# Kernel tuning notes

Measured on AMD Instinct MI355X. Metric: run time of the kernel, lower is better.

The kernel has to match this reference:

```python
import jax, jax.numpy as jnp
import numpy as np

NUM_EXPERTS = 8
IN_FEATURES = 1024
HIDDEN_FEATURES = 4096
OUT_FEATURES = 1024
TOKENS = 8192


def setup_inputs() -> dict:
    key = jax.random.key(0)
    k_x, k_idx, k_w1, k_w2, k_b1, k_b2 = jax.random.split(key, 6)
    x = jax.random.normal(k_x, (TOKENS, IN_FEATURES), dtype=jnp.float32)
    indices_s = jax.random.randint(k_idx, (TOKENS,), 0, NUM_EXPERTS, dtype=jnp.int64)
    # learned parameters (torch uses torch.rand; scaled for numeric sanity)
    weight1 = jax.random.normal(k_w1, (NUM_EXPERTS, IN_FEATURES, HIDDEN_FEATURES), dtype=jnp.float32) * 0.02
    weight2 = jax.random.normal(k_w2, (NUM_EXPERTS, HIDDEN_FEATURES, OUT_FEATURES), dtype=jnp.float32) * 0.02
    bias1 = jax.random.normal(k_b1, (NUM_EXPERTS, HIDDEN_FEATURES), dtype=jnp.float32) * 0.02
    bias2 = jax.random.normal(k_b2, (NUM_EXPERTS, IN_FEATURES), dtype=jnp.float32) * 0.02
    return {"x": x, "indices_s": indices_s, "weight1": weight1, "weight2": weight2, "bias1": bias1, "bias2": bias2}


def reference(x, indices_s, weight1, weight2, bias1, bias2):
    # Per-token expert MLP. Rather than gathering full weight matrices per
    # token (weight[indices_s] -> [T, in, hid], huge), loop over the small
    # fixed expert set and mask-combine. Math identical to the torch module.
    T = x.shape[0]
    num_experts = weight1.shape[0]
    out = jnp.zeros((T, weight2.shape[2]), dtype=x.dtype)
    for e in range(num_experts):
        mask = (indices_s == e)[:, None]  # [T, 1]
        h = jax.nn.gelu(x @ weight1[e] + bias1[e], approximate=False)  # [T, hid]
        y = h @ weight2[e] + bias2[e]  # [T, out]
        out = out + jnp.where(mask, y, jnp.zeros((), dtype=x.dtype))
    # original returns shape [T, 1, out] (x was unsqueezed)
    return out[:, None, :]
```

## Files before the change

kernel.cpp:

```cpp
#include <hip/hip_runtime.h>
#include <hip/hip_bf16.h>
#include <math.h>

#define TOKENS 8192
#define IN_F   1024
#define HID_F  4096
#define OUT_F  1024
#define NEXP   8
#define TSLOTS 40

typedef __attribute__((ext_vector_type(8))) short bf16x8;
typedef __attribute__((ext_vector_type(4))) float f32x4;
typedef __attribute__((ext_vector_type(8))) unsigned short u16x8;

__device__ __forceinline__ unsigned short f2bf(float f) {
    unsigned int u = __float_as_uint(f);
    u += 0x7fffu + ((u >> 16) & 1u);
    return (unsigned short)(u >> 16);
}

__device__ __forceinline__ void gload_lds16(const unsigned short* g, unsigned char* lds) {
    __builtin_amdgcn_global_load_lds(
        (const __attribute__((address_space(1))) void*)g,
        (__attribute__((address_space(3))) void*)lds, 16, 0, 0);
}

__global__ void sort_kernel(const int* __restrict__ idx, int* __restrict__ perm,
                            int* __restrict__ off, int* __restrict__ table) {
    __shared__ int cnt[NEXP];
    __shared__ int base[NEXP];
    const int tid = threadIdx.x, lane = tid & 63;
    if (tid < NEXP) cnt[tid] = 0;
    __syncthreads();
    for (int i = tid; i < TOKENS; i += 1024) {
        int e = idx[i];
#pragma unroll
        for (int ex = 0; ex < NEXP; ++ex) {
            unsigned long long m = __ballot(e == ex);
            if (lane == 0 && m) atomicAdd(&cnt[ex], __popcll(m));
        }
    }
    __syncthreads();
    if (tid == 0) {
        int s = 0;
        for (int e = 0; e < NEXP; ++e) { off[e] = s; base[e] = s; s += cnt[e]; }
        off[NEXP] = s;
        int t = 0;
        for (int e = 0; e < NEXP; ++e)
            for (int m0 = off[e]; m0 < off[e + 1]; m0 += 256)
                table[t++] = (e << 13) | m0;
        for (; t < TSLOTS; ++t) table[t] = -1;
    }
    __syncthreads();
    for (int i = tid; i < TOKENS; i += 1024) {
        int e = idx[i];
#pragma unroll
        for (int ex = 0; ex < NEXP; ++ex) {
            unsigned long long m = __ballot(e == ex);
            if (e == ex) {
                int lead = (int)__ffsll((long long)m) - 1;
                int pos = 0;
                if (lane == lead) pos = atomicAdd(&base[ex], __popcll(m));
                pos = __shfl(pos, lead);
                pos += __popcll(m & ((1ULL << lane) - 1ULL));
                perm[pos] = i;
            }
        }
    }
}

__device__ __forceinline__ void transp_tile(const float* __restrict__ in,
                                            unsigned short* __restrict__ out,
                                            int R, int C, int e, int by, int bx,
                                            unsigned short* T, int st) {
    const int r0 = by * 64, c0 = bx * 64;
    const int rr = st >> 4, cc = st & 15;
    const float* ip = in + ((size_t)e * R + r0) * C + c0;
#pragma unroll
    for (int p = 0; p < 4; ++p) {
        int r = p * 16 + rr;
        float4 v = *(const float4*)(ip + (size_t)r * C + cc * 4);
        T[(cc * 4 + 0) * 65 + r] = f2bf(v.x);
        T[(cc * 4 + 1) * 65 + r] = f2bf(v.y);
        T[(cc * 4 + 2) * 65 + r] = f2bf(v.z);
        T[(cc * 4 + 3) * 65 + r] = f2bf(v.w);
    }
    __syncthreads();
    unsigned short* op = out + ((size_t)e * C + c0) * R + r0;
    const int c = st >> 2, ch = st & 3;
    u16x8 a, b;
#pragma unroll
    for (int i = 0; i < 8; ++i) a[i] = T[c * 65 + ch * 16 + i];
#pragma unroll
    for (int i = 0; i < 8; ++i) b[i] = T[c * 65 + ch * 16 + 8 + i];
    *(u16x8*)(op + (size_t)c * R + ch * 16) = a;
    *(u16x8*)(op + (size_t)c * R + ch * 16 + 8) = b;
}

__global__ void transp(const float* __restrict__ in, unsigned short* __restrict__ out,
                       int R, int C) {
    __shared__ unsigned short T[64 * 65];
    transp_tile(in, out, R, C, blockIdx.z, blockIdx.y, blockIdx.x, T, threadIdx.x);
}

__global__ void fused_pre(const float* __restrict__ x, const int* __restrict__ perm,
                          unsigned short* __restrict__ xg,
                          const float* __restrict__ w1, unsigned short* __restrict__ w1t) {
    __shared__ unsigned short T[64 * 65];
    const int bid = blockIdx.x, t = threadIdx.x;
    if (bid < TOKENS) {
        const int src = perm[bid];
        float4 v = *(const float4*)(x + (size_t)src * IN_F + t * 4);
        unsigned long long pk =
            (unsigned long long)f2bf(v.x) |
            ((unsigned long long)f2bf(v.y) << 16) |
            ((unsigned long long)f2bf(v.z) << 32) |
            ((unsigned long long)f2bf(v.w) << 48);
        *(unsigned long long*)(xg + (size_t)bid * IN_F + t * 4) = pk;
        return;
    }
    const int id = bid - TOKENS;
    const int e = id >> 10, rem = id & 1023;
    const int by = rem >> 6, bx = rem & 63;
    transp_tile(w1, w1t, IN_F, HID_F, e, by, bx, T, t);
}

#define RD_A(RB, HALF) \
  _Pragma("unroll") for (int m_ = 0; m_ < 4; ++m_) { \
    const int row_ = wr * 128 + (HALF) * 64 + m_ * 16 + lr; \
    _Pragma("unroll") for (int kk_ = 0; kk_ < 2; ++kk_) \
      aR[m_][kk_] = *(const bf16x8*)((RB) + row_ * 128 + (((kk_ * 4 + hk) << 4) ^ xorc)); }

#define RD_B(RB, NH, DST) \
  _Pragma("unroll") for (int nn_ = 0; nn_ < 2; ++nn_) { \
    const int row_ = wc * 64 + ((NH) * 2 + nn_) * 16 + lr; \
    _Pragma("unroll") for (int kk_ = 0; kk_ < 2; ++kk_) \
      DST[nn_][kk_] = *(const bf16x8*)((RB) + 32768 + row_ * 128 + (((kk_ * 4 + hk) << 4) ^ xorc)); }

#define MFMA_Q(MH, NH, B) \
  __builtin_amdgcn_s_setprio(1); \
  _Pragma("unroll") for (int m_ = 0; m_ < 4; ++m_) \
    _Pragma("unroll") for (int nn_ = 0; nn_ < 2; ++nn_) \
      _Pragma("unroll") for (int kk_ = 0; kk_ < 2; ++kk_) \
        acc[(MH) * 4 + m_][(NH) * 2 + nn_] = __builtin_amdgcn_mfma_f32_16x16x32_bf16( \
            aR[m_][kk_], B[nn_][kk_], acc[(MH) * 4 + m_][(NH) * 2 + nn_], 0, 0, 0); \
  __builtin_amdgcn_s_setprio(0);

template<int K, int ND, bool GELU>
__launch_bounds__(512, 2)
__global__ void moe_gemm8p(const unsigned short* __restrict__ A,
                           const unsigned short* __restrict__ W,
                           const float* __restrict__ bias,
                           const int* __restrict__ perm,
                           const int* __restrict__ off,
                           const int* __restrict__ table,
                           void* __restrict__ outp,
                           const float* __restrict__ w2src,
                           unsigned short* __restrict__ w2t) {
    const int nwg = (ND / 256) * TSLOTS;

    __shared__ __align__(16) unsigned char L[131072];
    const int tid = threadIdx.x;

    if ((int)blockIdx.x >= nwg) {
        const int sub = tid >> 8, st = tid & 255;
        const int id2 = ((int)blockIdx.x - nwg) * 2 + sub;
        const int e = id2 >> 10, rem = id2 & 1023;
        const int by = rem >> 4, bx = rem & 15;
        unsigned short* T = (unsigned short*)(L + sub * 8448);
        transp_tile(w2src, w2t, HID_F, OUT_F, e, by, bx, T, st);
        return;
    }

    const int chunk = nwg >> 3;
    const int logical = ((int)blockIdx.x & 7) * chunk + ((int)blockIdx.x >> 3);
    const int nt = logical / TSLOTS;
    const int ts = logical - nt * TSLOTS;
    const int te = table[ts];
    if (te < 0) return;
    const int e  = te >> 13;
    const int m0 = te & 8191;
    const int sege = off[e + 1];
    const int n0 = nt * 256;

    const int wid = tid >> 6, lane = tid & 63;
    const int wr = wid >> 2, wc = wid & 3;
    const int lr = lane & 15, hk = lane >> 4;

    const unsigned short* We = W + (size_t)e * ND * K + (size_t)n0 * K;

    const int srow8 = lane >> 3;
    const int sch   = (lane & 7) ^ srow8;
    const unsigned short* aSrc[4];
    const unsigned short* wSrc[4];
#pragma unroll
    for (int cc = 0; cc < 4; ++cc) {
        int rt = cc * 64 + wid * 8 + srow8;
        int ga = m0 + rt; if (ga > TOKENS - 1) ga = TOKENS - 1;
        aSrc[cc] = A  + (size_t)ga * K + sch * 8;
        wSrc[cc] = We + (size_t)rt * K + sch * 8;
    }
    const int dstBase = wid * 1024;

    constexpr int NT = K / 64;

    auto stageH = [&](int tile, int h) {
        const int buf = (tile & 1) * 65536;
        const int op  = (h >> 1) * 32768;
        const int c0_ = (h & 1) * 2;
        const int ko  = tile * 64;
#pragma unroll
        for (int j = 0; j < 2; ++j) {
            int cc = c0_ + j;
            const unsigned short* s = (h < 2) ? (aSrc[cc] + ko) : (wSrc[cc] + ko);
            gload_lds16(s, L + buf + op + cc * 8192 + dstBase);
        }
    };

    f32x4 acc[8][4];
#pragma unroll
    for (int i = 0; i < 8; ++i)
#pragma unroll
        for (int j = 0; j < 4; ++j) acc[i][j] = (f32x4){0.f, 0.f, 0.f, 0.f};

    bf16x8 aR[4][2], b0R[2][2], b1R[2][2];
    const int xorc = (lr & 7) << 4;
    const unsigned char* rb0 = L;
    const unsigned char* rb1 = L + 65536;

    stageH(0, 0); stageH(0, 1); stageH(0, 2); stageH(0, 3);
    stageH(1, 0);
    asm volatile("s_waitcnt vmcnt(2)" ::: "memory");
    __builtin_amdgcn_s_barrier();
    __builtin_amdgcn_sched_barrier(0);

#pragma unroll 1
    for (int i = 0; i < NT / 2; ++i) {
        const int T1 = 2 * i + 1;
        const bool lastIt = (i == NT / 2 - 1);
        RD_A(rb0, 0); RD_B(rb0, 0, b0R);
        stageH(T1, 1);
        __builtin_amdgcn_s_barrier();
        MFMA_Q(0, 0, b0R);
        __builtin_amdgcn_s_barrier();
        RD_B(rb0, 1, b1R);
        stageH(T1, 2);
        __builtin_amdgcn_s_barrier();
        MFMA_Q(0, 1, b1R);
        __builtin_amdgcn_s_barrier();
        RD_A(rb0, 1);
        stageH(T1, 3);
        __builtin_amdgcn_s_barrier();
        MFMA_Q(1, 1, b1R);
        __builtin_amdgcn_s_barrier();
        if (!lastIt) stageH(T1 + 1, 0);
        __builtin_amdgcn_s_barrier();
        MFMA_Q(1, 0, b0R);
        if (lastIt) { asm volatile("s_waitcnt vmcnt(0)" ::: "memory"); }
        else        { asm volatile("s_waitcnt vmcnt(2)" ::: "memory"); }
        __builtin_amdgcn_s_barrier();
        __builtin_amdgcn_sched_barrier(0);
        RD_A(rb1, 0); RD_B(rb1, 0, b0R);
        if (!lastIt) stageH(T1 + 1, 1);
        __builtin_amdgcn_s_barrier();
        MFMA_Q(0, 0, b0R);
        __builtin_amdgcn_s_barrier();
        RD_B(rb1, 1, b1R);
        if (!lastIt) stageH(T1 + 1, 2);
        __builtin_amdgcn_s_barrier();
        MFMA_Q(0, 1, b1R);
        __builtin_amdgcn_s_barrier();
        RD_A(rb1, 1);
        if (!lastIt) stageH(T1 + 1, 3);
        __builtin_amdgcn_s_barrier();
        MFMA_Q(1, 1, b1R);
        __builtin_amdgcn_s_barrier();
        if (!lastIt) stageH(T1 + 2, 0);
        __builtin_amdgcn_s_barrier();
        MFMA_Q(1, 0, b0R);
        if (!lastIt) { asm volatile("s_waitcnt vmcnt(2)" ::: "memory"); }
        __builtin_amdgcn_s_barrier();
        __builtin_amdgcn_sched_barrier(0);
    }

    const float* be = bias + (size_t)e * ND + n0;
#pragma unroll
    for (int m = 0; m < 8; ++m) {
#pragma unroll
        for (int r = 0; r < 4; ++r) {
            int row = wr * 128 + m * 16 + hk * 4 + r;
            int grow = m0 + row;
            if (grow >= sege) continue;
            if constexpr (GELU) {
                unsigned short* h = (unsigned short*)outp;
                size_t base = (size_t)grow * ND + n0;
#pragma unroll
                for (int n = 0; n < 4; ++n) {
                    int col = wc * 64 + n * 16 + lr;
                    float v = acc[m][n][r] + be[col];
                    float u = v * (0.7978845608f + 0.0356774081f * v * v);
                    float g = v / (1.0f + __expf(-2.0f * u));
                    h[base + col] = f2bf(g);
                }
            } else {
                float* out = (float*)outp;
                int tok = perm[grow];
                size_t base = (size_t)tok * ND + n0;
#pragma unroll
                for (int n = 0; n < 4; ++n) {
                    int col = wc * 64 + n * 16 + lr;
                    out[base + col] = acc[m][n][r] + be[col];
                }
            }
        }
    }
}

extern "C" void kernel_launch(void* const* d_in, const int* in_sizes, int n_in,
                              void* d_out, int out_size, void* d_ws, size_t ws_size,
                              hipStream_t stream) {
    const float* x   = (const float*)d_in[0];
    const int*   idx = (const int*)d_in[1];
    const float* w1  = (const float*)d_in[2];
    const float* w2  = (const float*)d_in[3];
    const float* b1  = (const float*)d_in[4];
    const float* b2  = (const float*)d_in[5];
    float* out = (float*)d_out;

    int* perm  = (int*)d_ws;
    int* off   = perm + TOKENS;
    int* table = off + 16;
    unsigned short* xg  = (unsigned short*)((char*)d_ws + 65536);
    unsigned short* h   = xg + (size_t)TOKENS * IN_F;
    unsigned short* w1t = h + (size_t)TOKENS * HID_F;
    unsigned short* w2t = w1t + (size_t)NEXP * IN_F * HID_F;
    const size_t need_fused = 65536
        + (size_t)TOKENS * IN_F * 2
        + (size_t)TOKENS * HID_F * 2
        + (size_t)NEXP * IN_F * HID_F * 2 * 2;
    const bool fused = (ws_size >= need_fused);

    hipLaunchKernelGGL(sort_kernel, dim3(1), dim3(1024), 0, stream, idx, perm, off, table);
    hipLaunchKernelGGL(fused_pre, dim3(TOKENS + NEXP * (IN_F / 64) * (HID_F / 64)),
                       dim3(256), 0, stream, x, perm, xg, w1, w1t);

    const int g1 = (HID_F / 256) * TSLOTS;
    const int t2 = NEXP * (OUT_F / 64) * (HID_F / 64) / 2;
    if (fused) {
        hipLaunchKernelGGL((moe_gemm8p<IN_F, HID_F, true>), dim3(g1 + t2), dim3(512),
                           0, stream, xg, w1t, b1, perm, off, table, (void*)h, w2, w2t);
        hipLaunchKernelGGL((moe_gemm8p<HID_F, OUT_F, false>),
                           dim3((OUT_F / 256) * TSLOTS), dim3(512),
                           0, stream, h, w2t, b2, perm, off, table, (void*)out,
                           (const float*)nullptr, (unsigned short*)nullptr);
    } else {
        hipLaunchKernelGGL((moe_gemm8p<IN_F, HID_F, true>), dim3(g1), dim3(512),
                           0, stream, xg, w1t, b1, perm, off, table, (void*)h,
                           (const float*)nullptr, (unsigned short*)nullptr);
        hipLaunchKernelGGL(transp, dim3(OUT_F / 64, HID_F / 64, NEXP), dim3(256), 0, stream,
                           w2, w1t, HID_F, OUT_F);
        hipLaunchKernelGGL((moe_gemm8p<HID_F, OUT_F, false>),
                           dim3((OUT_F / 256) * TSLOTS), dim3(512),
                           0, stream, h, w1t, b2, perm, off, table, (void*)out,
                           (const float*)nullptr, (unsigned short*)nullptr);
    }
}
```

Before: 320.0 us.

## Merge MoE pipeline into persistent cooperative kernel with grid syncs and smaller GEMM2 tiles

Replaces the separate pre-processing, GEMM1 and GEMM2 launches with one persistent cooperative kernel of 256 workgroups. Each workgroup pulls work items from atomic counters, and grid-wide syncs separate the three phases. GEMM2 moves to 128x128 tiles with a new table, giving more tiles so the work is better balanced across CUs. Launch gaps and tail imbalance shrink, at the cost of occupancy 1 (512 threads, 128KB LDS), grid-sync overhead and lost overlap between phases. A fallback path using standalone kernels runs if the cooperative launch fails.

Result: slower. 797.8 us (+149.3%).

```diff
diff --git a/kernel.cpp b/kernel.cpp
--- a/kernel.cpp
+++ b/kernel.cpp
@@ -1,13 +1,17 @@
 #include <hip/hip_runtime.h>
 #include <hip/hip_bf16.h>
+#include <hip/hip_cooperative_groups.h>
 #include <math.h>
+
+namespace cg = cooperative_groups;
 
 #define TOKENS 8192
 #define IN_F   1024
 #define HID_F  4096
 #define OUT_F  1024
 #define NEXP   8
-#define TSLOTS 40
+#define TSLOTS    40
+#define TSLOTS128 72
 
 typedef __attribute__((ext_vector_type(8))) short bf16x8;
 typedef __attribute__((ext_vector_type(4))) float f32x4;
@@ -26,7 +30,8 @@
 }
 
 __global__ void sort_kernel(const int* __restrict__ idx, int* __restrict__ perm,
-                            int* __restrict__ off, int* __restrict__ table) {
+                            int* __restrict__ off, int* __restrict__ table,
+                            int* __restrict__ table128, int* __restrict__ ctrs) {
     __shared__ int cnt[NEXP];
     __shared__ int base[NEXP];
     const int tid = threadIdx.x, lane = tid & 63;
@@ -50,6 +55,12 @@
             for (int m0 = off[e]; m0 < off[e + 1]; m0 += 256)
                 table[t++] = (e << 13) | m0;
         for (; t < TSLOTS; ++t) table[t] = -1;
+        int t2 = 0;
+        for (int e = 0; e < NEXP; ++e)
+            for (int m0 = off[e]; m0 < off[e + 1]; m0 += 128)
+                table128[t2++] = (e << 13) | m0;
+        for (; t2 < TSLOTS128; ++t2) table128[t2] = -1;
+        ctrs[0] = 0; ctrs[1] = 0; ctrs[2] = 0; ctrs[3] = 0;
     }
     __syncthreads();
     for (int i = tid; i < TOKENS; i += 1024) {
@@ -95,12 +106,6 @@
     for (int i = 0; i < 8; ++i) b[i] = T[c * 65 + ch * 16 + 8 + i];
     *(u16x8*)(op + (size_t)c * R + ch * 16) = a;
     *(u16x8*)(op + (size_t)c * R + ch * 16 + 8) = b;
-}
-
-__global__ void transp(const float* __restrict__ in, unsigned short* __restrict__ out,
-                       int R, int C) {
-    __shared__ unsigned short T[64 * 65];
-    transp_tile(in, out, R, C, blockIdx.z, blockIdx.y, blockIdx.x, T, threadIdx.x);
 }
 
 __global__ void fused_pre(const float* __restrict__ x, const int* __restrict__ perm,
@@ -120,9 +125,7 @@
         return;
     }
     const int id = bid - TOKENS;
-    const int e = id >> 10, rem = id & 1023;
-    const int by = rem >> 6, bx = rem & 63;
-    transp_tile(w1, w1t, IN_F, HID_F, e, by, bx, T, t);
+    transp_tile(w1, w1t, IN_F, HID_F, id >> 10, (id >> 6) & 15, id & 63, T, t);
 }
 
 #define RD_A(RB, HALF) \
@@ -146,49 +149,18 @@
             aR[m_][kk_], B[nn_][kk_], acc[(MH) * 4 + m_][(NH) * 2 + nn_], 0, 0, 0); \
   __builtin_amdgcn_s_setprio(0);
 
-template<int K, int ND, bool GELU>
-__launch_bounds__(512, 2)
-__global__ void moe_gemm8p(const unsigned short* __restrict__ A,
+template<int K, int ND>
+__device__ void gemm1_tile(const unsigned short* __restrict__ A,
                            const unsigned short* __restrict__ W,
                            const float* __restrict__ bias,
-                           const int* __restrict__ perm,
-                           const int* __restrict__ off,
-                           const int* __restrict__ table,
-                           void* __restrict__ outp,
-                           const float* __restrict__ w2src,
-                           unsigned short* __restrict__ w2t) {
-    const int nwg = (ND / 256) * TSLOTS;
-
-    __shared__ __align__(16) unsigned char L[131072];
-    const int tid = threadIdx.x;
-
-    if ((int)blockIdx.x >= nwg) {
-        const int sub = tid >> 8, st = tid & 255;
-        const int id2 = ((int)blockIdx.x - nwg) * 2 + sub;
-        const int e = id2 >> 10, rem = id2 & 1023;
-        const int by = rem >> 4, bx = rem & 15;
-        unsigned short* T = (unsigned short*)(L + sub * 8448);
-        transp_tile(w2src, w2t, HID_F, OUT_F, e, by, bx, T, st);
-        return;
-    }
-
-    const int chunk = nwg >> 3;
-    const int logical = ((int)blockIdx.x & 7) * chunk + ((int)blockIdx.x >> 3);
-    const int nt = logical / TSLOTS;
-    const int ts = logical - nt * TSLOTS;
-    const int te = table[ts];
-    if (te < 0) return;
-    const int e  = te >> 13;
-    const int m0 = te & 8191;
-    const int sege = off[e + 1];
-    const int n0 = nt * 256;
-
+                           unsigned short* __restrict__ hout,
+                           int e, int m0, int sege, int n0,
+                           unsigned char* L, int tid) {
     const int wid = tid >> 6, lane = tid & 63;
     const int wr = wid >> 2, wc = wid & 3;
     const int lr = lane & 15, hk = lane >> 4;
 
     const unsigned short* We = W + (size_t)e * ND * K + (size_t)n0 * K;
-
     const int srow8 = lane >> 3;
     const int sch   = (lane & 7) ^ srow8;
     const unsigned short* aSrc[4];
@@ -201,7 +173,6 @@
         wSrc[cc] = We + (size_t)rt * K + sch * 8;
     }
     const int dstBase = wid * 1024;
-
     constexpr int NT = K / 64;
 
     auto stageH = [&](int tile, int h) {
@@ -291,29 +262,232 @@
             int row = wr * 128 + m * 16 + hk * 4 + r;
             int grow = m0 + row;
             if (grow >= sege) continue;
-            if constexpr (GELU) {
-                unsigned short* h = (unsigned short*)outp;
-                size_t base = (size_t)grow * ND + n0;
-#pragma unroll
-                for (int n = 0; n < 4; ++n) {
-                    int col = wc * 64 + n * 16 + lr;
-                    float v = acc[m][n][r] + be[col];
-                    float u = v * (0.7978845608f + 0.0356774081f * v * v);
-                    float g = v / (1.0f + __expf(-2.0f * u));
-                    h[base + col] = f2bf(g);
-                }
-            } else {
-                float* out = (float*)outp;
-                int tok = perm[grow];
-                size_t base = (size_t)tok * ND + n0;
-#pragma unroll
-                for (int n = 0; n < 4; ++n) {
-                    int col = wc * 64 + n * 16 + lr;
-                    out[base + col] = acc[m][n][r] + be[col];
-                }
+            size_t base = (size_t)grow * ND + n0;
+#pragma unroll
+            for (int n = 0; n < 4; ++n) {
+                int col = wc * 64 + n * 16 + lr;
+                float v = acc[m][n][r] + be[col];
+                float u = v * (0.7978845608f + 0.0356774081f * v * v);
+                float g = v / (1.0f + __expf(-2.0f * u));
+                hout[base + col] = f2bf(g);
             }
         }
     }
+}
+
+__device__ void gemm2_tile(const unsigned short* __restrict__ A,
+                           const unsigned short* __restrict__ Wt,
+                           const float* __restrict__ bias,
+                           const int* __restrict__ perm,
+                           float* __restrict__ out,
+                           int e, int m0, int sege, int n0,
+                           unsigned char* L, int tid) {
+    const int wid = tid >> 6, lane = tid & 63;
+    const int wr = wid >> 1, wc = wid & 1;
+    const int lr = lane & 15, hk = lane >> 4;
+    constexpr int K = HID_F, NT = K / 64;
+
+    const unsigned short* We = Wt + (size_t)e * OUT_F * K + (size_t)n0 * K;
+    const int srow8 = lane >> 3;
+    const int sch   = (lane & 7) ^ srow8;
+    const unsigned short* aSrc[2];
+    const unsigned short* wSrc[2];
+#pragma unroll
+    for (int cc = 0; cc < 2; ++cc) {
+        int rt = cc * 64 + wid * 8 + srow8;
+        int ga = m0 + rt; if (ga > TOKENS - 1) ga = TOKENS - 1;
+        aSrc[cc] = A  + (size_t)ga * K + sch * 8;
+        wSrc[cc] = We + (size_t)rt * K + sch * 8;
+    }
+    const int dstBase = wid * 1024;
+
+    auto stageP = [&](int tile, int part) {
+        const int buf = (tile & 1) * 32768;
+        const int o   = part * 8192;
+        const int cc  = part & 1;
+        const unsigned short* s = (part < 2) ? (aSrc[cc] + tile * 64)
+                                             : (wSrc[cc] + tile * 64);
+        gload_lds16(s, L + buf + o + dstBase);
+    };
+
+    f32x4 acc[2][4];
+#pragma unroll
+    for (int i = 0; i < 2; ++i)
+#pragma unroll
+        for (int j = 0; j < 4; ++j) acc[i][j] = (f32x4){0.f, 0.f, 0.f, 0.f};
+
+    const int xorc = (lr & 7) << 4;
+
+    stageP(0, 0); stageP(0, 1); stageP(0, 2); stageP(0, 3);
+    stageP(1, 0);
+
+#pragma unroll 1
+    for (int t = 0; t < NT; ++t) {
+        if (t == NT - 1) { asm volatile("s_waitcnt vmcnt(0)" ::: "memory"); }
+        else             { asm volatile("s_waitcnt vmcnt(1)" ::: "memory"); }
+        __builtin_amdgcn_s_barrier();
+        __builtin_amdgcn_sched_barrier(0);
+        const unsigned char* rb = L + (t & 1) * 32768;
+        bf16x8 a2[2][2], b2r[4][2];
+#pragma unroll
+        for (int m = 0; m < 2; ++m) {
+            int row = wr * 32 + m * 16 + lr;
+#pragma unroll
+            for (int kk = 0; kk < 2; ++kk)
+                a2[m][kk] = *(const bf16x8*)(rb + row * 128 + (((kk * 4 + hk) << 4) ^ xorc));
+        }
+#pragma unroll
+        for (int n = 0; n < 4; ++n) {
+            int row = wc * 64 + n * 16 + lr;
+#pragma unroll
+            for (int kk = 0; kk < 2; ++kk)
+                b2r[n][kk] = *(const bf16x8*)(rb + 16384 + row * 128 + (((kk * 4 + hk) << 4) ^ xorc));
+        }
+        if (t + 1 < NT) { stageP(t + 1, 1); stageP(t + 1, 2); stageP(t + 1, 3); }
+        __builtin_amdgcn_s_setprio(1);
+#pragma unroll
+        for (int m = 0; m < 2; ++m)
+#pragma unroll
+            for (int n = 0; n < 4; ++n)
+#pragma unroll
+                for (int kk = 0; kk < 2; ++kk)
+                    acc[m][n] = __builtin_amdgcn_mfma_f32_16x16x32_bf16(a2[m][kk], b2r[n][kk], acc[m][n], 0, 0, 0);
+        __builtin_amdgcn_s_setprio(0);
+        __builtin_amdgcn_s_barrier();
+        if (t + 2 < NT) stageP(t + 2, 0);
+    }
+
+    const float* be = bias + (size_t)e * OUT_F + n0;
+#pragma unroll
+    for (int m = 0; m < 2; ++m) {
+#pragma unroll
+        for (int r = 0; r < 4; ++r) {
+            int row = wr * 32 + m * 16 + hk * 4 + r;
+            int grow = m0 + row;
+            if (grow >= sege) continue;
+            int tok = perm[grow];
+            size_t base = (size_t)tok * OUT_F + n0;
+#pragma unroll
+            for (int n = 0; n < 4; ++n) {
+                int col = wc * 64 + n * 16 + lr;
+                out[base + col] = acc[m][n][r] + be[col];
+            }
+        }
+    }
+}
+
+__global__ __launch_bounds__(512, 1)
+void moe_mega(const float* __restrict__ x, const int* __restrict__ perm,
+              const int* __restrict__ off, const int* __restrict__ table,
+              const int* __restrict__ table128, int* __restrict__ ctrs,
+              unsigned short* __restrict__ xg, const float* __restrict__ w1,
+              unsigned short* __restrict__ w1t, const float* __restrict__ w2,
+              unsigned short* __restrict__ w2t, unsigned short* __restrict__ h,
+              const float* __restrict__ b1, const float* __restrict__ b2,
+              float* __restrict__ out) {
+    __shared__ __align__(16) unsigned char L[131072];
+    __shared__ int wslot;
+    const int tid = threadIdx.x;
+
+    for (;;) {
+        if (tid == 0) wslot = atomicAdd(&ctrs[0], 1);
+        __syncthreads();
+        const int t = wslot;
+        __syncthreads();
+        if (t >= 8192) break;
+        if (t < 4096) {
+            const int row = t * 2 + (tid >> 8);
+            const int c = tid & 255;
+            const int src = perm[row];
+            float4 v = *(const float4*)(x + (size_t)src * IN_F + c * 4);
+            unsigned long long pk =
+                (unsigned long long)f2bf(v.x) |
+                ((unsigned long long)f2bf(v.y) << 16) |
+                ((unsigned long long)f2bf(v.z) << 32) |
+                ((unsigned long long)f2bf(v.w) << 48);
+            *(unsigned long long*)(xg + (size_t)row * IN_F + c * 4) = pk;
+        } else {
+            const int id = (t - 4096) * 2 + (tid >> 8);
+            transp_tile(w1, w1t, IN_F, HID_F, id >> 10, (id >> 6) & 15, id & 63,
+                        (unsigned short*)(L + (tid >> 8) * 8448), tid & 255);
+        }
+    }
+    __threadfence();
+    cg::this_grid().sync();
+
+    for (;;) {
+        if (tid == 0) wslot = atomicAdd(&ctrs[1], 1);
+        __syncthreads();
+        const int t = wslot;
+        __syncthreads();
+        if (t >= 640 + 4096) break;
+        if (t < 640) {
+            const int nt = t / TSLOTS, ts = t - nt * TSLOTS;
+            const int te = table[ts];
+            if (te < 0) continue;
+            const int e = te >> 13;
+            gemm1_tile<IN_F, HID_F>(xg, w1t, b1, h, e, te & 8191, off[e + 1],
+                                    nt * 256, L, tid);
+        } else {
+            const int id2 = (t - 640) * 2 + (tid >> 8);
+            transp_tile(w2, w2t, HID_F, OUT_F, id2 >> 10, (id2 >> 4) & 63, id2 & 15,
+                        (unsigned short*)(L + (tid >> 8) * 8448), tid & 255);
+        }
+    }
+    __threadfence();
+    cg::this_grid().sync();
+
+    for (;;) {
+        if (tid == 0) wslot = atomicAdd(&ctrs[2], 1);
+        __syncthreads();
+        const int t = wslot;
+        __syncthreads();
+        if (t >= NEXP * TSLOTS128) break;
+        const int nt = t / TSLOTS128, ts = t - nt * TSLOTS128;
+        const int te = table128[ts];
+        if (te < 0) continue;
+        const int e = te >> 13;
+        gemm2_tile(h, w2t, b2, perm, out, e, te & 8191, off[e + 1],
+                   nt * 128, L, tid);
+    }
+}
+
+__global__ __launch_bounds__(512, 1)
+void moe_gemm1_sa(const unsigned short* __restrict__ A, const unsigned short* __restrict__ W,
+                  const float* __restrict__ bias, const int* __restrict__ off,
+                  const int* __restrict__ table, unsigned short* __restrict__ hout,
+                  const float* __restrict__ w2src, unsigned short* __restrict__ w2t) {
+    __shared__ __align__(16) unsigned char L[131072];
+    const int tid = threadIdx.x;
+    const int nwg = (HID_F / 256) * TSLOTS;
+    if ((int)blockIdx.x >= nwg) {
+        const int sub = tid >> 8, st = tid & 255;
+        const int id2 = ((int)blockIdx.x - nwg) * 2 + sub;
+        transp_tile(w2src, w2t, HID_F, OUT_F, id2 >> 10, (id2 >> 4) & 63, id2 & 15,
+                    (unsigned short*)(L + sub * 8448), st);
+        return;
+    }
+    const int chunk = nwg >> 3;
+    const int logical = ((int)blockIdx.x & 7) * chunk + ((int)blockIdx.x >> 3);
+    const int nt = logical / TSLOTS, ts = logical - nt * TSLOTS;
+    const int te = table[ts];
+    if (te < 0) return;
+    const int e = te >> 13;
+    gemm1_tile<IN_F, HID_F>(A, W, bias, hout, e, te & 8191, off[e + 1], nt * 256, L, tid);
+}
+
+__global__ __launch_bounds__(512, 1)
+void moe_gemm2_sa(const unsigned short* __restrict__ h, const unsigned short* __restrict__ w2t,
+                  const float* __restrict__ b2, const int* __restrict__ perm,
+                  const int* __restrict__ off, const int* __restrict__ table128,
+                  float* __restrict__ out) {
+    __shared__ __align__(16) unsigned char L[131072];
+    const int nt = (int)blockIdx.x / TSLOTS128;
+    const int ts = (int)blockIdx.x - nt * TSLOTS128;
+    const int te = table128[ts];
+    if (te < 0) return;
+    const int e = te >> 13;
+    gemm2_tile(h, w2t, b2, perm, out, e, te & 8191, off[e + 1], nt * 128, L, threadIdx.x);
 }
 
 extern "C" void kernel_launch(void* const* d_in, const int* in_sizes, int n_in,
@@ -327,41 +501,33 @@
     const float* b2  = (const float*)d_in[5];
     float* out = (float*)d_out;
 
-    int* perm  = (int*)d_ws;
-    int* off   = perm + TOKENS;
-    int* table = off + 16;
+    int* perm     = (int*)d_ws;
+    int* off      = perm + TOKENS;
+    int* table    = off + 16;
+    int* table128 = table + 64;
+    int* ctrs     = table128 + 80;
     unsigned short* xg  = (unsigned short*)((char*)d_ws + 65536);
     unsigned short* h   = xg + (size_t)TOKENS * IN_F;
     unsigned short* w1t = h + (size_t)TOKENS * HID_F;
     unsigned short* w2t = w1t + (size_t)NEXP * IN_F * HID_F;
-    const size_t need_fused = 65536
-        + (size_t)TOKENS * IN_F * 2
-        + (size_t)TOKENS * HID_F * 2
-        + (size_t)NEXP * IN_F * HID_F * 2 * 2;
-    const bool fused = (ws_size >= need_fused);
-
-    hipLaunchKernelGGL(sort_kernel, dim3(1), dim3(1024), 0, stream, idx, perm, off, table);
-    hipLaunchKernelGGL(fused_pre, dim3(TOKENS + NEXP * (IN_F / 64) * (HID_F / 64)),
-                       dim3(256), 0, stream, x, perm, xg, w1, w1t);
-
-    const int g1 = (HID_F / 256) * TSLOTS;
-    const int t2 = NEXP * (OUT_F / 64) * (HID_F / 64) / 2;
-    if (fused) {
-        hipLaunchKernelGGL((moe_gemm8p<IN_F, HID_F, true>), dim3(g1 + t2), dim3(512),
-                           0, stream, xg, w1t, b1, perm, off, table, (void*)h, w2, w2t);
-        hipLaunchKernelGGL((moe_gemm8p<HID_F, OUT_F, false>),
-                           dim3((OUT_F / 256) * TSLOTS), dim3(512),
-                           0, stream, h, w2t, b2, perm, off, table, (void*)out,
-                           (const float*)nullptr, (unsigned short*)nullptr);
-    } else {
-        hipLaunchKernelGGL((moe_gemm8p<IN_F, HID_F, true>), dim3(g1), dim3(512),
-                           0, stream, xg, w1t, b1, perm, off, table, (void*)h,
-                           (const float*)nullptr, (unsigned short*)nullptr);
-        hipLaunchKernelGGL(transp, dim3(OUT_F / 64, HID_F / 64, NEXP), dim3(256), 0, stream,
-                           w2, w1t, HID_F, OUT_F);
-        hipLaunchKernelGGL((moe_gemm8p<HID_F, OUT_F, false>),
-                           dim3((OUT_F / 256) * TSLOTS), dim3(512),
-                           0, stream, h, w1t, b2, perm, off, table, (void*)out,
-                           (const float*)nullptr, (unsigned short*)nullptr);
-    }
-}
+
+    hipLaunchKernelGGL(sort_kernel, dim3(1), dim3(1024), 0, stream,
+                       idx, perm, off, table, table128, ctrs);
+
+    void* args[] = { (void*)&x, (void*)&perm, (void*)&off, (void*)&table,
+                     (void*)&table128, (void*)&ctrs, (void*)&xg, (void*)&w1,
+                     (void*)&w1t, (void*)&w2, (void*)&w2t, (void*)&h,
+                     (void*)&b1, (void*)&b2, (void*)&out };
+    hipError_t err = hipLaunchCooperativeKernel((const void*)moe_mega,
+                                                dim3(256), dim3(512), args, 0, stream);
+    if (err != hipSuccess) {
+        hipLaunchKernelGGL(fused_pre, dim3(TOKENS + NEXP * (IN_F / 64) * (HID_F / 64)),
+                           dim3(256), 0, stream, x, perm, xg, w1, w1t);
+        const int g1 = (HID_F / 256) * TSLOTS;
+        const int t2 = NEXP * (OUT_F / 64) * (HID_F / 64) / 2;
+        hipLaunchKernelGGL(moe_gemm1_sa, dim3(g1 + t2), dim3(512), 0, stream,
+                           xg, w1t, b1, off, table, h, w2, w2t);
+        hipLaunchKernelGGL(moe_gemm2_sa, dim3(NEXP * TSLOTS128), dim3(512), 0, stream,
+                           h, w2t, b2, perm, off, table128, out);
+    }
+}
```
